# Kernel tuning notes

Hardware: AMD Instinct MI355X
Metric: run time of the kernel (lower is better)

The kernel has to match this reference:

```python
import jax, jax.numpy as jnp
import numpy as np


def setup_inputs() -> dict:
    key = jax.random.key(0)
    ks = jax.random.split(key, 8)
    B, N, D, Fn, Fe = 16, 512, 64, 32, 1
    return {
        "prev_embeddings": jax.random.normal(ks[0], (B, N, D), dtype=jnp.float32),
        "adj": jax.random.uniform(ks[1], (B, N, N), dtype=jnp.float32),
        "node_features": jax.random.normal(ks[2], (B, N, Fn), dtype=jnp.float32),
        "edge_features": jax.random.uniform(ks[3], (B, N, N), dtype=jnp.float32),
        "W1": jax.random.normal(ks[4], (Fn, D), dtype=jnp.float32) * (1.0 / np.sqrt(Fn)),
        "W2": jax.random.normal(ks[5], (D, D), dtype=jnp.float32) * (1.0 / np.sqrt(D)),
        "W3": jax.random.normal(ks[6], (D, D), dtype=jnp.float32) * (1.0 / np.sqrt(D)),
        "W4": jax.random.normal(ks[7], (Fe, D), dtype=jnp.float32),
    }


def reference(prev_embeddings, adj, node_features, edge_features, W1, W2, W3, W4):
    # x1 = theta1(node_features): (B,N,D)
    x1 = jnp.einsum("bnf,fd->bnd", node_features, W1)
    # x2 = theta2(adj @ prev): (B,N,D)
    x2 = jnp.einsum("bij,bjd,de->bie", adj, prev_embeddings, W2)
    # edge_features (B,N,N) -> (B,N,N,1); x4 = relu(theta4(e)): (B,N,N,D)
    e = edge_features[..., None]
    x4 = jax.nn.relu(jnp.einsum("bijf,fd->bijd", e, W4))
    # adjacency-weighted sum over neighbors j: (B,N,D)
    s = jnp.einsum("bij,bijd->bid", adj, x4)
    x3 = jnp.einsum("bid,de->bie", s, W3)
    return jax.nn.relu(x1 + x2 + x3)
```

## Files before the change

kernel.cpp:

```cpp
#include <hip/hip_runtime.h>

#define BATCH 16
#define NN    512
#define DD    64
#define FN    32
#define HALF  256
#define CHUNK 128

__global__ __launch_bounds__(256) void aggregate_kernel(
    const float* __restrict__ prev,
    const float* __restrict__ adj,
    const float* __restrict__ ef,
    float* __restrict__ apbuf,
    float* __restrict__ tbuf)
{
    __shared__ float prevS[CHUNK * DD];

    const int tid  = threadIdx.x;
    const int lane = tid & 63;
    const int w    = __builtin_amdgcn_readfirstlane(tid >> 6);
    const int bi   = blockIdx.x;
    const int h    = bi & 1;
    const int g    = (bi >> 1) & 15;
    const int b    = bi >> 5;
    const int i0   = g * 32 + w * 8;
    const int jb   = h * HALF;

    float t[8];
    #pragma unroll
    for (int r = 0; r < 8; ++r) {
        const int rowo = (b * NN + i0 + r) * NN + jb;
        float4 a = ((const float4*)(adj + rowo))[lane];
        float4 e = ((const float4*)(ef  + rowo))[lane];
        float tp = a.x * e.x + a.y * e.y + a.z * e.z + a.w * e.w;
        #pragma unroll
        for (int s = 1; s < 64; s <<= 1) tp += __shfl_xor(tp, s, 64);
        t[r] = tp;
    }

    float acc[8] = {0.f,0.f,0.f,0.f,0.f,0.f,0.f,0.f};
    const float* pb = prev + b * NN * DD + jb * DD;

    for (int c = 0; c < 2; ++c) {
        const float4* src = (const float4*)(pb + c * CHUNK * DD);
        float4* dst = (float4*)prevS;
        #pragma unroll
        for (int it = 0; it < 8; ++it)
            dst[it * 256 + tid] = src[it * 256 + tid];
        __syncthreads();

        const float* a_base = adj + (b * NN + i0) * NN + jb + c * CHUNK;
        #pragma unroll 4
        for (int j = 0; j < CHUNK; ++j) {
            float pv = prevS[j * DD + lane];
            #pragma unroll
            for (int r = 0; r < 8; ++r)
                acc[r] = fmaf(a_base[r * NN + j], pv, acc[r]);
        }
        __syncthreads();
    }

    #pragma unroll
    for (int r = 0; r < 8; ++r) {
        const int row = b * NN + i0 + r;
        apbuf[(h * BATCH * NN + row) * DD + lane] = acc[r];
        if (lane == 0) tbuf[h * BATCH * NN + row] = t[r];
    }
}

__global__ __launch_bounds__(256) void epilogue_kernel(
    const float* __restrict__ apbuf,
    const float* __restrict__ tbuf,
    const float* __restrict__ nf,
    const float* __restrict__ W1,
    const float* __restrict__ W2,
    const float* __restrict__ W3,
    const float* __restrict__ W4,
    float* __restrict__ out)
{
    const int tid  = threadIdx.x;
    const int lane = tid & 63;
    const int w    = __builtin_amdgcn_readfirstlane(tid >> 6);
    const int row0 = blockIdx.x * 16 + w * 4;

    float w2c[DD];
    #pragma unroll
    for (int k = 0; k < DD; ++k) w2c[k] = W2[k * DD + lane];
    float w1c[FN];
    #pragma unroll
    for (int f = 0; f < FN; ++f) w1c[f] = W1[f * DD + lane];

    float v3 = 0.f;
    #pragma unroll
    for (int d = 0; d < DD; ++d)
        v3 = fmaf(fmaxf(W4[d], 0.f), W3[d * DD + lane], v3);

    #pragma unroll
    for (int r = 0; r < 4; ++r) {
        const int row = row0 + r;
        float ap = apbuf[row * DD + lane]
                 + apbuf[(BATCH * NN + row) * DD + lane];
        float tv = tbuf[row] + tbuf[BATCH * NN + row];
        float acc = tv * v3;
        #pragma unroll
        for (int k = 0; k < DD; ++k) {
            float a = __int_as_float(
                __builtin_amdgcn_readlane(__float_as_int(ap), k));
            acc = fmaf(a, w2c[k], acc);
        }
        const float* nrow = nf + row * FN;
        #pragma unroll
        for (int f = 0; f < FN; ++f)
            acc = fmaf(nrow[f], w1c[f], acc);
        out[row * DD + lane] = fmaxf(acc, 0.f);
    }
}

extern "C" void kernel_launch(void* const* d_in, const int* in_sizes, int n_in,
                              void* d_out, int out_size, void* d_ws, size_t ws_size,
                              hipStream_t stream) {
    const float* prev = (const float*)d_in[0];
    const float* adj  = (const float*)d_in[1];
    const float* nf   = (const float*)d_in[2];
    const float* ef   = (const float*)d_in[3];
    const float* W1   = (const float*)d_in[4];
    const float* W2   = (const float*)d_in[5];
    const float* W3   = (const float*)d_in[6];
    const float* W4   = (const float*)d_in[7];
    float* out = (float*)d_out;

    float* apbuf = (float*)d_ws;
    float* tbuf  = apbuf + 2 * BATCH * NN * DD;

    aggregate_kernel<<<dim3(512), dim3(256), 0, stream>>>(prev, adj, ef, apbuf, tbuf);
    epilogue_kernel<<<dim3(512), dim3(256), 0, stream>>>(apbuf, tbuf, nf, W1, W2, W3, W4, out);
}
```

Baseline: 116.8 us.

## Convert inputs to bf16 and compute aggregation and projections with MFMA

Replaces both kernels. A prep kernel converts adj, prev (transposed), node features and weights to bf16 while computing the edge term. A single-wave MFMA GEMM kernel then computes adj@prev and fuses the W1/W2 projections, bias term and relu. This moves the FP32 FMA-bound aggregation onto matrix cores, at the cost of an extra bf16 write/read of adj and reduced precision.

```diff
diff --git a/kernel.cpp b/kernel.cpp
--- a/kernel.cpp
+++ b/kernel.cpp
@@ -1,119 +1,166 @@
 #include <hip/hip_runtime.h>
 
-#define BATCH 16
-#define NN    512
-#define DD    64
-#define FN    32
-#define HALF  256
-#define CHUNK 128
+#define NN 512
+#define DD 64
+#define FN 32
+#define NROWS 8192
 
-__global__ __launch_bounds__(256) void aggregate_kernel(
-    const float* __restrict__ prev,
-    const float* __restrict__ adj,
-    const float* __restrict__ ef,
-    float* __restrict__ apbuf,
+typedef unsigned short ushortT;
+typedef __attribute__((ext_vector_type(4))) unsigned short us4;
+typedef __attribute__((ext_vector_type(8))) short s8;
+typedef __attribute__((ext_vector_type(4))) float f4;
+
+__device__ inline ushortT f2bf(float x) {
+    unsigned u = __float_as_uint(x);
+    return (ushortT)((u + 0x7FFFu + ((u >> 16) & 1u)) >> 16);
+}
+
+__global__ __launch_bounds__(256) void prep_kernel(
+    const float* __restrict__ prev, const float* __restrict__ adj,
+    const float* __restrict__ nf,   const float* __restrict__ ef,
+    const float* __restrict__ W1,   const float* __restrict__ W2,
+    const float* __restrict__ W3,   const float* __restrict__ W4,
+    ushortT* __restrict__ adjb, ushortT* __restrict__ prevT,
+    ushortT* __restrict__ nfb,  ushortT* __restrict__ W1T,
+    ushortT* __restrict__ W2T,  float* __restrict__ v3,
     float* __restrict__ tbuf)
 {
-    __shared__ float prevS[CHUNK * DD];
+    const int bk = blockIdx.x, tid = threadIdx.x;
 
-    const int tid  = threadIdx.x;
-    const int lane = tid & 63;
-    const int w    = __builtin_amdgcn_readfirstlane(tid >> 6);
-    const int bi   = blockIdx.x;
-    const int h    = bi & 1;
-    const int g    = (bi >> 1) & 15;
-    const int b    = bi >> 5;
-    const int i0   = g * 32 + w * 8;
-    const int jb   = h * HALF;
+    if (bk < 512) {
+        const int lane = tid & 63, w = tid >> 6;
+        const int row0 = bk * 16 + w * 4;
+        #pragma unroll
+        for (int r = 0; r < 4; ++r) {
+            const int row = row0 + r;
+            const float4* a4 = (const float4*)(adj + row * NN);
+            const float4* e4 = (const float4*)(ef  + row * NN);
+            float4 a0 = a4[lane], a1 = a4[64 + lane];
+            float4 e0 = e4[lane], e1 = e4[64 + lane];
+            float tp = a0.x*e0.x + a0.y*e0.y + a0.z*e0.z + a0.w*e0.w
+                     + a1.x*e1.x + a1.y*e1.y + a1.z*e1.z + a1.w*e1.w;
+            #pragma unroll
+            for (int s = 1; s < 64; s <<= 1) tp += __shfl_xor(tp, s, 64);
+            us4 o0 = { f2bf(a0.x), f2bf(a0.y), f2bf(a0.z), f2bf(a0.w) };
+            us4 o1 = { f2bf(a1.x), f2bf(a1.y), f2bf(a1.z), f2bf(a1.w) };
+            ((us4*)(adjb + row * NN))[lane]      = o0;
+            ((us4*)(adjb + row * NN))[64 + lane] = o1;
+            if (lane == 0) tbuf[row] = tp;
+        }
+    } else if (bk < 528) {
+        __shared__ float T[64][65];
+        const int b = bk - 512;
+        for (int c = 0; c < 8; ++c) {
+            #pragma unroll
+            for (int s = 0; s < 16; ++s) {
+                int idx = s * 256 + tid;
+                int jl = idx >> 6, d = idx & 63;
+                T[jl][d] = prev[b * NN * DD + (c * 64 + jl) * DD + d];
+            }
+            __syncthreads();
+            #pragma unroll
+            for (int s = 0; s < 16; ++s) {
+                int idx = s * 256 + tid;
+                int d = idx >> 6, jl = idx & 63;
+                prevT[b * DD * NN + d * NN + c * 64 + jl] = f2bf(T[jl][d]);
+            }
+            __syncthreads();
+        }
+    } else if (bk < 592) {
+        const int base = (bk - 528) * 4096;
+        #pragma unroll
+        for (int s = 0; s < 4; ++s) {
+            int i = base + s * 1024 + tid * 4;
+            float4 v = *(const float4*)(nf + i);
+            us4 o = { f2bf(v.x), f2bf(v.y), f2bf(v.z), f2bf(v.w) };
+            *(us4*)(nfb + i) = o;
+        }
+    } else {
+        for (int i = tid; i < DD * FN; i += 256) {
+            int e = i >> 5, f = i & 31;
+            W1T[i] = f2bf(W1[f * DD + e]);
+        }
+        for (int i = tid; i < DD * DD; i += 256) {
+            int e = i >> 6, d = i & 63;
+            W2T[i] = f2bf(W2[d * DD + e]);
+        }
+        if (tid < DD) {
+            float s = 0.f;
+            for (int d = 0; d < DD; ++d)
+                s = fmaf(fmaxf(W4[d], 0.f), W3[d * DD + tid], s);
+            v3[tid] = s;
+        }
+    }
+}
 
-    float t[8];
+__global__ __launch_bounds__(64) void gemm_kernel(
+    const ushortT* __restrict__ adjb, const ushortT* __restrict__ prevT,
+    const ushortT* __restrict__ nfb,  const ushortT* __restrict__ W1T,
+    const ushortT* __restrict__ W2T,  const float* __restrict__ v3,
+    const float* __restrict__ tbuf,   float* __restrict__ out)
+{
+    __shared__ __align__(16) ushortT PT[16 * 72];
+
+    const int l   = threadIdx.x;
+    const int i0  = blockIdx.x * 16;
+    const int b   = i0 >> 9;
+    const int l15 = l & 15, g = l >> 4;
+
+    f4 zero = {0.f, 0.f, 0.f, 0.f};
+    f4 acc[4] = {zero, zero, zero, zero};
+    const ushortT* arow = adjb  + (i0 + l15) * NN + 8 * g;
+    const ushortT* pb   = prevT + b * DD * NN + l15 * NN + 8 * g;
+
     #pragma unroll
-    for (int r = 0; r < 8; ++r) {
-        const int rowo = (b * NN + i0 + r) * NN + jb;
-        float4 a = ((const float4*)(adj + rowo))[lane];
-        float4 e = ((const float4*)(ef  + rowo))[lane];
-        float tp = a.x * e.x + a.y * e.y + a.z * e.z + a.w * e.w;
+    for (int ks = 0; ks < 16; ++ks) {
+        s8 A = *(const s8*)(arow + 32 * ks);
         #pragma unroll
-        for (int s = 1; s < 64; s <<= 1) tp += __shfl_xor(tp, s, 64);
-        t[r] = tp;
-    }
-
-    float acc[8] = {0.f,0.f,0.f,0.f,0.f,0.f,0.f,0.f};
-    const float* pb = prev + b * NN * DD + jb * DD;
-
-    for (int c = 0; c < 2; ++c) {
-        const float4* src = (const float4*)(pb + c * CHUNK * DD);
-        float4* dst = (float4*)prevS;
-        #pragma unroll
-        for (int it = 0; it < 8; ++it)
-            dst[it * 256 + tid] = src[it * 256 + tid];
-        __syncthreads();
-
-        const float* a_base = adj + (b * NN + i0) * NN + jb + c * CHUNK;
-        #pragma unroll 4
-        for (int j = 0; j < CHUNK; ++j) {
-            float pv = prevS[j * DD + lane];
-            #pragma unroll
-            for (int r = 0; r < 8; ++r)
-                acc[r] = fmaf(a_base[r * NN + j], pv, acc[r]);
+        for (int nt = 0; nt < 4; ++nt) {
+            s8 B = *(const s8*)(pb + nt * 16 * NN + 32 * ks);
+            acc[nt] = __builtin_amdgcn_mfma_f32_16x16x32_bf16(A, B, acc[nt], 0, 0, 0);
         }
-        __syncthreads();
     }
 
     #pragma unroll
-    for (int r = 0; r < 8; ++r) {
-        const int row = b * NN + i0 + r;
-        apbuf[(h * BATCH * NN + row) * DD + lane] = acc[r];
-        if (lane == 0) tbuf[h * BATCH * NN + row] = t[r];
+    for (int nt = 0; nt < 4; ++nt)
+        #pragma unroll
+        for (int r = 0; r < 4; ++r)
+            PT[(4 * g + r) * 72 + 16 * nt + l15] = f2bf(acc[nt][r]);
+
+    float tr[4];
+    #pragma unroll
+    for (int r = 0; r < 4; ++r) tr[r] = tbuf[i0 + 4 * g + r];
+    f4 o[4];
+    #pragma unroll
+    for (int nt = 0; nt < 4; ++nt) {
+        float vv = v3[16 * nt + l15];
+        o[nt][0] = tr[0] * vv; o[nt][1] = tr[1] * vv;
+        o[nt][2] = tr[2] * vv; o[nt][3] = tr[3] * vv;
     }
-}
 
-__global__ __launch_bounds__(256) void epilogue_kernel(
-    const float* __restrict__ apbuf,
-    const float* __restrict__ tbuf,
-    const float* __restrict__ nf,
-    const float* __restrict__ W1,
-    const float* __restrict__ W2,
-    const float* __restrict__ W3,
-    const float* __restrict__ W4,
-    float* __restrict__ out)
-{
-    const int tid  = threadIdx.x;
-    const int lane = tid & 63;
-    const int w    = __builtin_amdgcn_readfirstlane(tid >> 6);
-    const int row0 = blockIdx.x * 16 + w * 4;
-
-    float w2c[DD];
+    s8 A1 = *(const s8*)(nfb + (i0 + l15) * FN + 8 * g);
     #pragma unroll
-    for (int k = 0; k < DD; ++k) w2c[k] = W2[k * DD + lane];
-    float w1c[FN];
-    #pragma unroll
-    for (int f = 0; f < FN; ++f) w1c[f] = W1[f * DD + lane];
-
-    float v3 = 0.f;
-    #pragma unroll
-    for (int d = 0; d < DD; ++d)
-        v3 = fmaf(fmaxf(W4[d], 0.f), W3[d * DD + lane], v3);
+    for (int nt = 0; nt < 4; ++nt) {
+        s8 B1 = *(const s8*)(W1T + (16 * nt + l15) * FN + 8 * g);
+        o[nt] = __builtin_amdgcn_mfma_f32_16x16x32_bf16(A1, B1, o[nt], 0, 0, 0);
+    }
 
     #pragma unroll
-    for (int r = 0; r < 4; ++r) {
-        const int row = row0 + r;
-        float ap = apbuf[row * DD + lane]
-                 + apbuf[(BATCH * NN + row) * DD + lane];
-        float tv = tbuf[row] + tbuf[BATCH * NN + row];
-        float acc = tv * v3;
+    for (int k2 = 0; k2 < 2; ++k2) {
+        s8 A2 = *(const s8*)(&PT[l15 * 72 + 32 * k2 + 8 * g]);
         #pragma unroll
-        for (int k = 0; k < DD; ++k) {
-            float a = __int_as_float(
-                __builtin_amdgcn_readlane(__float_as_int(ap), k));
-            acc = fmaf(a, w2c[k], acc);
+        for (int nt = 0; nt < 4; ++nt) {
+            s8 B2 = *(const s8*)(W2T + (16 * nt + l15) * DD + 32 * k2 + 8 * g);
+            o[nt] = __builtin_amdgcn_mfma_f32_16x16x32_bf16(A2, B2, o[nt], 0, 0, 0);
         }
-        const float* nrow = nf + row * FN;
+    }
+
+    float* orow = out + i0 * DD;
+    #pragma unroll
+    for (int nt = 0; nt < 4; ++nt)
         #pragma unroll
-        for (int f = 0; f < FN; ++f)
-            acc = fmaf(nrow[f], w1c[f], acc);
-        out[row * DD + lane] = fmaxf(acc, 0.f);
-    }
+        for (int r = 0; r < 4; ++r)
+            orow[(4 * g + r) * DD + 16 * nt + l15] = fmaxf(o[nt][r], 0.f);
 }
 
 extern "C" void kernel_launch(void* const* d_in, const int* in_sizes, int n_in,
@@ -129,9 +176,17 @@
     const float* W4   = (const float*)d_in[7];
     float* out = (float*)d_out;
 
-    float* apbuf = (float*)d_ws;
-    float* tbuf  = apbuf + 2 * BATCH * NN * DD;
+    char* ws = (char*)d_ws;
+    ushortT* adjb  = (ushortT*)(ws + 0);
+    ushortT* prevT = (ushortT*)(ws + 8388608);
+    ushortT* nfb   = (ushortT*)(ws + 9437184);
+    ushortT* W1T   = (ushortT*)(ws + 9961472);
+    ushortT* W2T   = (ushortT*)(ws + 9965568);
+    float*   v3    = (float*)  (ws + 9973760);
+    float*   tbuf  = (float*)  (ws + 9974016);
 
-    aggregate_kernel<<<dim3(512), dim3(256), 0, stream>>>(prev, adj, ef, apbuf, tbuf);
-    epilogue_kernel<<<dim3(512), dim3(256), 0, stream>>>(apbuf, tbuf, nf, W1, W2, W3, W4, out);
+    prep_kernel<<<dim3(593), dim3(256), 0, stream>>>(
+        prev, adj, nf, ef, W1, W2, W3, W4, adjb, prevT, nfb, W1T, W2T, v3, tbuf);
+    gemm_kernel<<<dim3(512), dim3(64), 0, stream>>>(
+        adjb, prevT, nfb, W1T, W2T, v3, tbuf, out);
 }
```

Result: faster. 102.3 us (-12.4%).
